# Performance work log

Hardware: AMD Instinct MI355X
Metric: run time of the kernel (lower is better)

The kernel has to match this reference:

```python
import jax, jax.numpy as jnp
import numpy as np

MARGIN = 0.3
WARMUP_EPOCHS = 10
K = 5
ALPHA = 2.0
SAME_CAM_NEG_BOOST = 1.2
NEG_INF = jnp.float32(-jnp.inf)
POS_INF = jnp.float32(jnp.inf)


def setup_inputs() -> dict:
    key = jax.random.key(0)
    k1, k2, k3 = jax.random.split(key, 3)
    N, D = 8192, 2048
    feats = jax.random.normal(k1, (N, D), dtype=jnp.float32)
    labels = jax.random.randint(k2, (N,), 0, 256, dtype=jnp.int64)
    camids = jax.random.randint(k3, (N,), 0, 8, dtype=jnp.int64)
    return {"feats": feats, "labels": labels, "camids": camids, "epoch": 20}


def _topk_mean(dist_mat, mask, k, largest):
    # dist_mat [N,N], mask [N,N] bool. Per-row mean of k largest/smallest valid elems.
    if largest:
        work = jnp.where(mask, dist_mat, NEG_INF)
        vals, _ = jax.lax.top_k(work, k)            # [N,k] largest
        fallback = jnp.max(work, axis=1)
    else:
        work = jnp.where(mask, dist_mat, POS_INF)
        vals = -jax.lax.top_k(-work, k)[0]          # [N,k] smallest
        fallback = jnp.min(work, axis=1)
    is_valid = jnp.isfinite(vals)
    safe_sum = jnp.sum(jnp.where(is_valid, vals, 0.0), axis=1)
    counts = jnp.maximum(is_valid.sum(axis=1), 1)
    mean = safe_sum / counts
    return jnp.where(is_valid.any(axis=1), mean, fallback)


def _forward(feats, labels, camids, epoch):
    # (1) L2 normalize
    norm = jnp.linalg.norm(feats, axis=-1, keepdims=True)
    x = feats / jnp.maximum(norm, 1e-12)
    # Euclidean distance matrix [N,N]
    sq = jnp.sum(x * x, axis=1)
    dist2 = sq[:, None] + sq[None, :] - 2.0 * (x @ x.T)
    dist = jnp.sqrt(jnp.maximum(dist2, 1e-12))
    # masks (constants w.r.t. grad)
    N = feats.shape[0]
    eye = jnp.eye(N, dtype=bool)
    same_label = labels[:, None] == labels[None, :]
    same_cam = camids[:, None] == camids[None, :]
    is_pos = same_label & ~eye & ~same_cam   # cross_cam_pos=True
    is_neg = ~same_label & ~eye
    # boosted same-camera negatives
    neg_bias = jnp.where(is_neg & same_cam, SAME_CAM_NEG_BOOST, 1.0)
    dist_neg_sel = dist / jnp.maximum(neg_bias, 1e-6)
    # (2) top-k hard mining
    d_ap = _topk_mean(dist, is_pos, K, largest=True)
    d_an = _topk_mean(dist_neg_sel, is_neg, K, largest=False)
    # (5) hardness-aware weighting (no grad)
    w = jax.lax.stop_gradient(jax.nn.sigmoid(ALPHA * (d_ap - d_an)))
    w = w / jnp.maximum(w.mean(), 1e-12)
    # (3) margin schedule
    if epoch is not None and epoch < WARMUP_EPOCHS:
        per_sample = jax.nn.softplus(-(d_an - d_ap))
    else:
        per_sample = jax.nn.relu(d_ap - d_an + MARGIN)  # MarginRankingLoss, y=1
    loss = jnp.mean(w * per_sample)
    return loss, jax.lax.stop_gradient(d_ap), jax.lax.stop_gradient(d_an)


def reference(feats, labels, camids, epoch):
    return _forward(feats, labels, camids, epoch)
```

## Files before the change

kernel.cpp:

```cpp
#include <hip/hip_runtime.h>
#include <hip/hip_bf16.h>
#include <stdint.h>

typedef float   floatx4  __attribute__((ext_vector_type(4)));
typedef float   floatx16 __attribute__((ext_vector_type(16)));
typedef int     intx4    __attribute__((ext_vector_type(4)));
typedef int     intx8    __attribute__((ext_vector_type(8)));
typedef _Float16 halfx8  __attribute__((ext_vector_type(8)));
typedef _Float16 halfx4  __attribute__((ext_vector_type(4)));
typedef _Float16 half2v  __attribute__((ext_vector_type(2)));

#define NROW 8192
#define NDIM 2048
#define BM 128
#define SLICE 64
#define NSLICE 32
#define NSTRIP 64
#define NOFF (NSTRIP*(NSTRIP-1)/2)
#define NTILE (NSTRIP*(NSTRIP+1)/2)
#define DT_LD 136
#define KL_SYM 64
#define SLOT_P 8
#define MERGE_BLOCKS 256
#define BOOST_INV 0.6944444444f

__device__ __forceinline__ void ins_desc(float (&a)[5], float v) {
#pragma unroll
    for (int k = 0; k < 5; ++k) { float hi = fmaxf(a[k], v); float lo = fminf(a[k], v); a[k] = hi; v = lo; }
}
__device__ __forceinline__ void ins_asc(float (&a)[5], float v) {
#pragma unroll
    for (int k = 0; k < 5; ++k) { float lo = fminf(a[k], v); float hi = fmaxf(a[k], v); a[k] = lo; v = hi; }
}

__device__ __forceinline__ int   h2bits(half2v v) { return __builtin_bit_cast(int, v); }
__device__ __forceinline__ half2v bits2h(int v)   { return __builtin_bit_cast(half2v, v); }
__device__ __forceinline__ void ins_desc2(half2v (&a)[5], half2v v) {
#pragma unroll
    for (int k = 0; k < 5; ++k) {
        half2v hi = __builtin_elementwise_max(a[k], v);
        half2v lo = __builtin_elementwise_min(a[k], v);
        a[k] = hi; v = lo;
    }
}
__device__ __forceinline__ void ins_asc2(half2v (&a)[5], half2v v) {
#pragma unroll
    for (int k = 0; k < 5; ++k) {
        half2v lo = __builtin_elementwise_min(a[k], v);
        half2v hi = __builtin_elementwise_max(a[k], v);
        a[k] = lo; v = hi;
    }
}

__device__ __forceinline__ void load_lds16(const void* g, void* l) {
    __builtin_amdgcn_global_load_lds((__attribute__((address_space(1))) void*)(void*)g,
                                     (__attribute__((address_space(3))) void*)l,
                                     16, 0, 0);
}

__global__ __launch_bounds__(256) void k_normalize(const float* __restrict__ feats,
                                                   unsigned char* __restrict__ xb,
                                                   float* __restrict__ sq) {
    const int lane = threadIdx.x & 63;
    const int row = (blockIdx.x << 2) + (threadIdx.x >> 6);
    const float* f = feats + (size_t)row * NDIM;
    float4 v[8];
    float ss = 0.f;
#pragma unroll
    for (int i = 0; i < 8; ++i) {
        v[i] = *(const float4*)(f + ((i << 6) + lane) * 4);
        ss += v[i].x * v[i].x + v[i].y * v[i].y + v[i].z * v[i].z + v[i].w * v[i].w;
    }
#pragma unroll
    for (int o = 32; o > 0; o >>= 1) ss += __shfl_xor(ss, o);
    float inv = 1.0f / fmaxf(sqrtf(ss), 1e-12f);
    if (lane == 0) sq[row] = ss * inv * inv;
    unsigned char* xo = xb + (size_t)row * NDIM;
#pragma unroll
    for (int i = 0; i < 8; ++i) {
        int w0 = __builtin_amdgcn_cvt_pk_fp8_f32(v[i].x * inv, v[i].y * inv, 0, false);
        w0     = __builtin_amdgcn_cvt_pk_fp8_f32(v[i].z * inv, v[i].w * inv, w0, true);
        *(int*)(xo + ((i << 6) + lane) * 4) = w0;
    }
}

__device__ __forceinline__ void scan_half_row_neg(const _Float16* Dt_,
        int srow, int shalf, float (&neg5)[5]) {
    const int s2 = 2 * (srow & 7);
    const int PINF2 = 0x7C007C00;
    half2v n5[5];
#pragma unroll
    for (int k = 0; k < 5; ++k) n5[k] = bits2h(PINF2);
#pragma unroll
    for (int c8 = 0; c8 < 8; ++c8) {
        const int pc = ((shalf * 8 + c8) + s2) & 15;
        intx4 v = *(const intx4*)(Dt_ + srow * DT_LD + pc * 8);
#pragma unroll
        for (int e = 0; e < 4; ++e) ins_asc2(n5, bits2h(v[e]));
    }
    half2v tn[5];
#pragma unroll
    for (int k = 0; k < 5; ++k)
        tn[k] = bits2h((int)__builtin_amdgcn_alignbit((unsigned)h2bits(n5[k]), (unsigned)h2bits(n5[k]), 16));
#pragma unroll
    for (int k = 0; k < 5; ++k) ins_asc2(n5, tn[k]);
#pragma unroll
    for (int k = 0; k < 5; ++k) neg5[k] = (float)n5[k][0];
}

__device__ __forceinline__ void emit_neg(float (&neg5)[5], int shalf,
        _Float16* negp, int gi, int slot) {
    float tn[5];
#pragma unroll
    for (int k = 0; k < 5; ++k) tn[k] = __shfl_xor(neg5[k], 1);
#pragma unroll
    for (int k = 0; k < 5; ++k) { if (tn[k] < neg5[4]) ins_asc(neg5, tn[k]); }
    if (shalf == 0) {
        const float PINF = __builtin_inff();
        halfx8 hn;
#pragma unroll
        for (int k = 0; k < 5; ++k) hn[k] = (_Float16)neg5[k];
        hn[5] = hn[6] = hn[7] = (_Float16)PINF;
        *(halfx8*)(negp + ((size_t)slot * NROW + gi) * SLOT_P) = hn;
    }
}

__global__ __launch_bounds__(256, 3) void k_gemm_sym(
        const unsigned char* __restrict__ xb, const float* __restrict__ sq,
        const int* __restrict__ labels, const int* __restrict__ camids,
        _Float16* __restrict__ negp) {
    __shared__ __align__(16) char smem[49152 + 2048];
    _Float16* Dt = (_Float16*)smem;
    float* sqr_s = (float*)(smem + 49152);
    float* sqc_s = sqr_s + BM;
    unsigned short* labcam_a = (unsigned short*)(sqc_s + BM);
    unsigned short* labcam_b = labcam_a + BM;

    const int tid = threadIdx.x;
    const int w = tid >> 6, lane = tid & 63;
    const int wm = w >> 1, wn = w & 1;

    int a, b;
    {
        int bx = blockIdx.x;
        int orig;
        if (bx < NOFF) orig = (bx & 7) * (NOFF / 8) + (bx >> 3);
        else orig = bx;
        if (orig < NOFF) {
            a = (int)((1.0f + sqrtf(8.0f * (float)orig + 1.0f)) * 0.5f);
            while (a * (a - 1) / 2 > orig) --a;
            while (a * (a + 1) / 2 <= orig) ++a;
            b = orig - a * (a - 1) / 2;
        } else {
            a = b = orig - NOFF;
        }
    }
    const int r0 = a * BM, c0 = b * BM;

    const int lr = lane >> 2;
    const int lc = (((lane & 3) - ((lane >> 3) & 3)) & 3) * 16;

    auto stage = [&](int buf, int koff) {
        char* Asb = smem + (buf << 14);
        char* Bsb = Asb + 8192;
#pragma unroll
        for (int q = 0; q < 2; ++q) {
            const int ra = w * 32 + q * 16;
            load_lds16(xb + (size_t)(r0 + ra + lr) * NDIM + koff + lc, Asb + ra * SLICE);
            load_lds16(xb + (size_t)(c0 + ra + lr) * NDIM + koff + lc, Bsb + ra * SLICE);
        }
    };

    if (tid < BM) {
        int gi = r0 + tid;
        sqr_s[tid] = sq[gi];
        labcam_a[tid] = (unsigned short)((labels[gi] << 4) | camids[gi]);
    } else {
        int t2 = tid - BM;
        int gj = c0 + t2;
        sqc_s[t2] = sq[gj];
        labcam_b[t2] = (unsigned short)((labels[gj] << 4) | camids[gj]);
    }

    stage(0, 0);
    stage(1, SLICE);

    const int srow = tid >> 1;
    const int shalf = tid & 1;

    const int m32 = lane & 31;
    const int hi = lane >> 5;
    const int key = (lane >> 1) & 3;
    const int p0 = ((2 * hi + key) & 3) * 16;
    const int p1 = ((2 * hi + 1 + key) & 3) * 16;

    floatx16 acc[2][2];
#pragma unroll
    for (int ti = 0; ti < 2; ++ti)
#pragma unroll
        for (int tj = 0; tj < 2; ++tj)
#pragma unroll
            for (int r = 0; r < 16; ++r) acc[ti][tj][r] = 0.f;

    int bc = 0;
    for (int s = 0; s < NSLICE; ++s) {
        if (s + 2 < NSLICE) {
            int bs = bc + 2; if (bs >= 3) bs -= 3;
            stage(bs, (s + 2) * SLICE);
        }
        if (s < NSLICE - 2)       asm volatile("s_waitcnt vmcnt(8)" ::: "memory");
        else if (s == NSLICE - 2) asm volatile("s_waitcnt vmcnt(4)" ::: "memory");
        else                      asm volatile("s_waitcnt vmcnt(0)" ::: "memory");
        __builtin_amdgcn_s_barrier();
        asm volatile("" ::: "memory");

        const char* Ab = smem + (bc << 14);
        const char* Bb = Ab + 8192;
        intx8 bf[2];
#pragma unroll
        for (int tj = 0; tj < 2; ++tj) {
            const char* bp = Bb + (wn * 64 + tj * 32 + m32) * SLICE;
            intx4 lo = *(const intx4*)(bp + p0);
            intx4 hi4 = *(const intx4*)(bp + p1);
            bf[tj] = __builtin_shufflevector(lo, hi4, 0, 1, 2, 3, 4, 5, 6, 7);
        }
        __builtin_amdgcn_s_setprio(1);
#pragma unroll
        for (int ti = 0; ti < 2; ++ti) {
            const char* ap = Ab + (wm * 64 + ti * 32 + m32) * SLICE;
            intx4 lo = *(const intx4*)(ap + p0);
            intx4 hi4 = *(const intx4*)(ap + p1);
            intx8 af = __builtin_shufflevector(lo, hi4, 0, 1, 2, 3, 4, 5, 6, 7);
            acc[ti][0] = __builtin_amdgcn_mfma_scale_f32_32x32x64_f8f6f4(
                af, bf[0], acc[ti][0], 0, 0, 0, 127, 0, 127);
            acc[ti][1] = __builtin_amdgcn_mfma_scale_f32_32x32x64_f8f6f4(
                af, bf[1], acc[ti][1], 0, 0, 0, 127, 0, 127);
        }
        __builtin_amdgcn_s_setprio(0);
        asm volatile("" ::: "memory");
        __builtin_amdgcn_s_barrier();
        asm volatile("" ::: "memory");
        bc = (bc + 1 == 3) ? 0 : bc + 1;
    }

    const float FINF = __builtin_inff();
#pragma unroll
    for (int ti = 0; ti < 2; ++ti) {
#pragma unroll
        for (int tj = 0; tj < 2; ++tj) {
            const int jl = wn * 64 + tj * 32 + m32;
            const float sj = sqc_s[jl];
            const int lb = (int)labcam_b[jl];
#pragma unroll
            for (int r = 0; r < 16; ++r) {
                const int il = wm * 64 + ti * 32 + (r & 3) + 8 * (r >> 2) + 4 * hi;
                float d2 = fmaxf(sqr_s[il] + sj - 2.0f * acc[ti][tj][r], 1e-12f);
                const int x = (int)labcam_a[il] ^ lb;
                float nv = (x & 15) ? d2 : d2 * BOOST_INV;
                nv = (x & 0xFFF0) ? nv : FINF;
                acc[ti][tj][r] = nv;
                const int pch = ((jl >> 3) + 2 * (il & 7)) & 15;
                Dt[il * DT_LD + (pch << 3) + (jl & 7)] = (_Float16)nv;
            }
        }
    }
    __syncthreads();

    float neg5[5];
    scan_half_row_neg(Dt, srow, shalf, neg5);
    emit_neg(neg5, shalf, negp, r0 + srow, b);

    if (a != b) {
        __syncthreads();
#pragma unroll
        for (int tj = 0; tj < 2; ++tj) {
#pragma unroll
            for (int ti = 0; ti < 2; ++ti) {
                const int jl = wn * 64 + tj * 32 + m32;
                const int cw2 = 2 * (jl & 7);
#pragma unroll
                for (int rq = 0; rq < 4; ++rq) {
                    const int base_row = wm * 64 + ti * 32 + 8 * rq + 4 * hi;
                    halfx4 h;
#pragma unroll
                    for (int e = 0; e < 4; ++e) h[e] = (_Float16)acc[ti][tj][rq * 4 + e];
                    const int pch = (((base_row >> 3) + cw2) & 15);
                    *(halfx4*)(Dt + jl * DT_LD + (pch << 3) + 4 * hi) = h;
                }
            }
        }
        __syncthreads();
        scan_half_row_neg(Dt, srow, shalf, neg5);
        emit_neg(neg5, shalf, negp, c0 + srow, a);
    }
}

__global__ __launch_bounds__(256) void k_pos(const unsigned char* __restrict__ xb,
        const float* __restrict__ sq, const int* __restrict__ labels,
        const int* __restrict__ camids, _Float16* __restrict__ posf) {
    __shared__ int mem[64];
    __shared__ unsigned short mlc[64];
    __shared__ float msq[64];
    __shared__ int cnt_s;
    __shared__ __align__(16) char stg[2][4096];
    __shared__ __align__(16) _Float16 D2[64][72];

    const int t = threadIdx.x, L = blockIdx.x;
    if (t == 0) cnt_s = 0;
    __syncthreads();
    for (int i = t; i < NROW; i += 256) {
        if (labels[i] == L) {
            int slot = atomicAdd(&cnt_s, 1);
            if (slot < 64) mem[slot] = i;
        }
    }
    __syncthreads();
    const int cnt = min(cnt_s, 64);
    if (t < 64) {
        if (t < cnt) {
            int gi = mem[t];
            mlc[t] = (unsigned short)((labels[gi] << 4) | camids[gi]);
            msq[t] = sq[gi];
        } else {
            mem[t] = 0; mlc[t] = 0xFFFF; msq[t] = 0.f;
        }
    }
    __syncthreads();

    const int w = t >> 6, lane = t & 63;
    const int wm = w >> 1, wn = w & 1;
    const int lr = lane >> 2;
    const int lcb = (((lane & 3) - ((lane >> 3) & 3)) & 3) * 16;
    const int m32 = lane & 31, hi = lane >> 5;
    const int key = (lane >> 1) & 3;
    const int p0 = ((2 * hi + key) & 3) * 16;
    const int p1 = ((2 * hi + 1 + key) & 3) * 16;
    const int myrow = mem[w * 16 + lr];

    auto pstage = [&](int buf, int koff) {
        load_lds16(xb + (size_t)myrow * NDIM + koff + lcb, &stg[buf][0] + w * 1024);
    };

    floatx16 acc;
#pragma unroll
    for (int r = 0; r < 16; ++r) acc[r] = 0.f;

    pstage(0, 0);
    __syncthreads();
    for (int s = 0; s < NSLICE; ++s) {
        if (s + 1 < NSLICE) pstage((s + 1) & 1, (s + 1) * SLICE);
        const char* Ab = &stg[s & 1][0];
        const char* ap = Ab + (wm * 32 + m32) * SLICE;
        intx4 alo = *(const intx4*)(ap + p0);
        intx4 ahi = *(const intx4*)(ap + p1);
        intx8 af = __builtin_shufflevector(alo, ahi, 0, 1, 2, 3, 4, 5, 6, 7);
        const char* bp = Ab + (wn * 32 + m32) * SLICE;
        intx4 blo = *(const intx4*)(bp + p0);
        intx4 bhi = *(const intx4*)(bp + p1);
        intx8 bf = __builtin_shufflevector(blo, bhi, 0, 1, 2, 3, 4, 5, 6, 7);
        acc = __builtin_amdgcn_mfma_scale_f32_32x32x64_f8f6f4(af, bf, acc, 0, 0, 0, 127, 0, 127);
        __syncthreads();
    }

    const float NINF = -__builtin_inff();
    {
        const int jl = wn * 32 + m32;
        const int lcj = (int)mlc[jl];
        const float sj = msq[jl];
#pragma unroll
        for (int r = 0; r < 16; ++r) {
            const int il = wm * 32 + (r & 3) + 8 * (r >> 2) + 4 * hi;
            float d2 = fmaxf(msq[il] + sj - 2.0f * acc[r], 1e-12f);
            const int x = (int)mlc[il] ^ lcj;
            bool posv = ((x & 0xFFF0) == 0) & ((x & 15) != 0);
            D2[il][jl] = posv ? (_Float16)d2 : (_Float16)NINF;
        }
    }
    __syncthreads();

    {
        const int prow = t >> 2, q = t & 3;
        const int NINF2 = 0xFC00FC00;
        half2v p5h[5];
#pragma unroll
        for (int k = 0; k < 5; ++k) p5h[k] = bits2h(NINF2);
        const _Float16* dp = &D2[prow][q * 16];
        intx4 v0 = *(const intx4*)dp;
        intx4 v1 = *(const intx4*)(dp + 8);
#pragma unroll
        for (int e = 0; e < 4; ++e) ins_desc2(p5h, bits2h(v0[e]));
#pragma unroll
        for (int e = 0; e < 4; ++e) ins_desc2(p5h, bits2h(v1[e]));
        half2v tp[5];
#pragma unroll
        for (int k = 0; k < 5; ++k)
            tp[k] = bits2h((int)__builtin_amdgcn_alignbit((unsigned)h2bits(p5h[k]), (unsigned)h2bits(p5h[k]), 16));
#pragma unroll
        for (int k = 0; k < 5; ++k) ins_desc2(p5h, tp[k]);
        float p5[5];
#pragma unroll
        for (int k = 0; k < 5; ++k) p5[k] = (float)p5h[k][0];
#pragma unroll
        for (int o = 1; o <= 2; o <<= 1) {
            float tq[5];
#pragma unroll
            for (int k = 0; k < 5; ++k) tq[k] = __shfl_xor(p5[k], o);
#pragma unroll
            for (int k = 0; k < 5; ++k) { if (tq[k] > p5[4]) ins_desc(p5, tq[k]); }
        }
        if (q == 0 && prow < cnt) {
            halfx8 hp;
#pragma unroll
            for (int k = 0; k < 5; ++k) hp[k] = (_Float16)p5[k];
            hp[5] = hp[6] = hp[7] = (_Float16)NINF;
            *(halfx8*)(posf + (size_t)mem[prow] * SLOT_P) = hp;
        }
    }
}

__global__ __launch_bounds__(256) void k_merge_sym(const _Float16* __restrict__ negp,
        const _Float16* __restrict__ posf, const int* __restrict__ epoch_p,
        float* __restrict__ out, float* __restrict__ wsum_p, float* __restrict__ wpsum_p) {
    const int t = threadIdx.x;
    const int rl = t & 31;
    const int sg = t >> 5;
    const int row = blockIdx.x * 32 + rl;
    const float NINF = -__builtin_inff(), PINF = __builtin_inff();
    float n5[5] = {PINF, PINF, PINF, PINF, PINF};
    const size_t rbase = (size_t)row * SLOT_P;
#pragma unroll
    for (int s = 0; s < 8; ++s) {
        const size_t off = (size_t)(sg * 8 + s) * ((size_t)NROW * SLOT_P) + rbase;
        halfx8 nv = *(const halfx8*)(negp + off);
#pragma unroll
        for (int e = 0; e < 8; ++e) { float f = (float)nv[e]; if (f < n5[4]) ins_asc(n5, f); }
    }
    __shared__ __align__(16) _Float16 ln[32][8][8];
    const int sw = (sg + rl) & 7;
    {
        halfx8 hn;
#pragma unroll
        for (int k = 0; k < 5; ++k) hn[k] = (_Float16)n5[k];
        hn[5] = hn[6] = hn[7] = (_Float16)PINF;
        *(halfx8*)&ln[rl][sw][0] = hn;
    }
    __syncthreads();
    if (t < 32) {
        float N5[5] = {PINF, PINF, PINF, PINF, PINF};
#pragma unroll
        for (int g = 0; g < 8; ++g) {
            halfx8 nv = *(const halfx8*)&ln[t][g][0];
#pragma unroll
            for (int e = 0; e < 8; ++e) { float f = (float)nv[e]; if (f < N5[4]) ins_asc(N5, f); }
        }
        const int orow = blockIdx.x * 32 + t;
        halfx8 pv = *(const halfx8*)(posf + (size_t)orow * SLOT_P);
        float s = 0.f; int c = 0;
#pragma unroll
        for (int k = 0; k < 5; ++k) { float f = (float)pv[k]; bool fin = (f > NINF); s += fin ? sqrtf(f) : 0.f; c += fin ? 1 : 0; }
        float d_ap = (c > 0) ? s / (float)c : NINF;
        s = 0.f; c = 0;
#pragma unroll
        for (int k = 0; k < 5; ++k) { bool fin = (N5[k] < PINF); s += fin ? sqrtf(N5[k]) : 0.f; c += fin ? 1 : 0; }
        float d_an = (c > 0) ? s / (float)c : PINF;

        out[1 + orow] = d_ap;
        out[1 + NROW + orow] = d_an;
        float diff = d_ap - d_an;
        float w0 = 1.0f / (1.0f + expf(-2.0f * diff));
        float p;
        if (*epoch_p < 10) {
            p = fmaxf(diff, 0.0f) + log1pf(expf(-fabsf(diff)));
        } else {
            p = fmaxf(diff + 0.3f, 0.0f);
        }
        float wp = w0 * p;
#pragma unroll
        for (int o = 16; o > 0; o >>= 1) { w0 += __shfl_down(w0, o, 32); wp += __shfl_down(wp, o, 32); }
        if (t == 0) { wsum_p[blockIdx.x] = w0; wpsum_p[blockIdx.x] = wp; }
    }
}

__global__ void k_finalize(const float* __restrict__ wsum_p, const float* __restrict__ wpsum_p,
                           float* __restrict__ out) {
    const int t = threadIdx.x;
    float sw  = wsum_p[t] + wsum_p[t + 64] + wsum_p[t + 128] + wsum_p[t + 192];
    float swp = wpsum_p[t] + wpsum_p[t + 64] + wpsum_p[t + 128] + wpsum_p[t + 192];
#pragma unroll
    for (int o = 32; o > 0; o >>= 1) { sw += __shfl_down(sw, o); swp += __shfl_down(swp, o); }
    if (t == 0) {
        float M = fmaxf(sw / (float)NROW, 1e-12f);
        out[0] = swp / ((float)NROW * M);
    }
}

extern "C" void kernel_launch(void* const* d_in, const int* in_sizes, int n_in,
                              void* d_out, int out_size, void* d_ws, size_t ws_size,
                              hipStream_t stream) {
    const float* feats  = (const float*)d_in[0];
    const int*   labels = (const int*)d_in[1];
    const int*   camids = (const int*)d_in[2];
    const int*   epoch  = (const int*)d_in[3];
    float* out = (float*)d_out;
    char* ws = (char*)d_ws;

    unsigned char* xb = (unsigned char*)ws;
    float* sq = (float*)(ws + 16777216);
    const size_t NEG_HALVES = (size_t)KL_SYM * NROW * SLOT_P;
    _Float16* negp = (_Float16*)(ws + 16777216 + 32768);
    _Float16* posf = negp + NEG_HALVES;
    float* wsum_p  = (float*)((char*)(posf + (size_t)NROW * SLOT_P));
    float* wpsum_p = wsum_p + MERGE_BLOCKS;

    k_normalize<<<NROW / 4, 256, 0, stream>>>(feats, xb, sq);
    k_pos<<<256, 256, 0, stream>>>(xb, sq, labels, camids, posf);
    k_gemm_sym<<<NTILE, 256, 0, stream>>>(xb, sq, labels, camids, negp);
    k_merge_sym<<<MERGE_BLOCKS, 256, 0, stream>>>(negp, posf, epoch, out, wsum_p, wpsum_p);
    k_finalize<<<1, 64, 0, stream>>>(wsum_p, wpsum_p, out);
}
```

Before: 227.0 us.

## Fuse positive-pair kernel into symmetric GEMM launch and regroup tiles into 8x8 supertiles

Merges the per-label positive mining kernel into the main symmetric distance GEMM kernel as 256 extra leading blocks, which removes one launch and lets both kinds of work run concurrently. The tile index mapping now groups the 128x128 tiles into 8x8 supertiles, with diagonal supertiles handled separately, to improve L2 reuse of the row strips. The positive path switches to a 3-buffer pipeline with vmcnt waits, and the neg epilogue is restructured to share row loads across the two column subtiles. The cost is that the fused kernel runs at the larger shared-memory footprint and launch bounds of the GEMM path for every block.

```diff
diff --git a/kernel.cpp b/kernel.cpp
--- a/kernel.cpp
+++ b/kernel.cpp
@@ -16,8 +16,8 @@
 #define SLICE 64
 #define NSLICE 32
 #define NSTRIP 64
-#define NOFF (NSTRIP*(NSTRIP-1)/2)
 #define NTILE (NSTRIP*(NSTRIP+1)/2)
+#define NPOSB 256
 #define DT_LD 136
 #define KL_SYM 64
 #define SLOT_P 8
@@ -125,34 +125,181 @@
     }
 }
 
-__global__ __launch_bounds__(256, 3) void k_gemm_sym(
+__global__ __launch_bounds__(256, 3) void k_main(
         const unsigned char* __restrict__ xb, const float* __restrict__ sq,
         const int* __restrict__ labels, const int* __restrict__ camids,
-        _Float16* __restrict__ negp) {
-    __shared__ __align__(16) char smem[49152 + 2048];
+        _Float16* __restrict__ negp, _Float16* __restrict__ posf) {
+    __shared__ __align__(16) char smem[51200];
+
+    const int tid = threadIdx.x;
+    const int w = tid >> 6, lane = tid & 63;
+    const int m32 = lane & 31;
+    const int hi = lane >> 5;
+    const int key = (lane >> 1) & 3;
+    const int p0 = ((2 * hi + key) & 3) * 16;
+    const int p1 = ((2 * hi + 1 + key) & 3) * 16;
+    const float FINF = __builtin_inff();
+    const float NINF = -FINF;
+
+    if (blockIdx.x < NPOSB) {
+        char* stg0 = smem;
+        _Float16* D2 = (_Float16*)(smem + 12288);
+        int* mem = (int*)(smem + 21504);
+        unsigned short* mlc = (unsigned short*)(smem + 21760);
+        float* msq = (float*)(smem + 21888);
+        int* cntp = (int*)(smem + 22144);
+
+        const int L = blockIdx.x;
+        if (tid == 0) *cntp = 0;
+        __syncthreads();
+        for (int i = tid; i < NROW; i += 256) {
+            if (labels[i] == L) {
+                int slot = atomicAdd(cntp, 1);
+                if (slot < 64) mem[slot] = i;
+            }
+        }
+        __syncthreads();
+        const int cnt = min(*cntp, 64);
+        if (tid < 64) {
+            if (tid < cnt) {
+                int gi = mem[tid];
+                mlc[tid] = (unsigned short)((labels[gi] << 4) | camids[gi]);
+                msq[tid] = sq[gi];
+            } else {
+                mem[tid] = 0; mlc[tid] = 0xFFFF; msq[tid] = 0.f;
+            }
+        }
+        __syncthreads();
+
+        const int wm = w >> 1, wn = w & 1;
+        const int lr = lane >> 2;
+        const int lcb = (((lane & 3) - ((lane >> 3) & 3)) & 3) * 16;
+        const int myrow = mem[w * 16 + lr];
+
+        auto pstage = [&](int buf, int koff) {
+            load_lds16(xb + (size_t)myrow * NDIM + koff + lcb,
+                       stg0 + (buf << 12) + w * 1024);
+        };
+
+        floatx16 acc;
+#pragma unroll
+        for (int r = 0; r < 16; ++r) acc[r] = 0.f;
+
+        pstage(0, 0);
+        pstage(1, SLICE);
+        for (int s = 0; s < NSLICE; ++s) {
+            if (s + 2 < NSLICE) {
+                int bs = s + 2; bs -= (bs >= 3 ? 3 : 0); bs -= (bs >= 3 ? 3 : 0);
+                pstage((s + 2) % 3, (s + 2) * SLICE);
+            }
+            if (s < NSLICE - 2)       asm volatile("s_waitcnt vmcnt(2)" ::: "memory");
+            else if (s == NSLICE - 2) asm volatile("s_waitcnt vmcnt(1)" ::: "memory");
+            else                      asm volatile("s_waitcnt vmcnt(0)" ::: "memory");
+            __builtin_amdgcn_s_barrier();
+            asm volatile("" ::: "memory");
+            const char* Ab = stg0 + ((s % 3) << 12);
+            const char* ap = Ab + (wm * 32 + m32) * SLICE;
+            intx4 alo = *(const intx4*)(ap + p0);
+            intx4 ahi = *(const intx4*)(ap + p1);
+            intx8 af = __builtin_shufflevector(alo, ahi, 0, 1, 2, 3, 4, 5, 6, 7);
+            const char* bp = Ab + (wn * 32 + m32) * SLICE;
+            intx4 blo = *(const intx4*)(bp + p0);
+            intx4 bhi = *(const intx4*)(bp + p1);
+            intx8 bf = __builtin_shufflevector(blo, bhi, 0, 1, 2, 3, 4, 5, 6, 7);
+            acc = __builtin_amdgcn_mfma_scale_f32_32x32x64_f8f6f4(af, bf, acc, 0, 0, 0, 127, 0, 127);
+            asm volatile("" ::: "memory");
+            __builtin_amdgcn_s_barrier();
+            asm volatile("" ::: "memory");
+        }
+
+        {
+            const int jl = (w & 1) * 32 + m32;
+            const int lcj = (int)mlc[jl];
+            const float sj = msq[jl];
+            const int wm2 = w >> 1;
+#pragma unroll
+            for (int r = 0; r < 16; ++r) {
+                const int il = wm2 * 32 + (r & 3) + 8 * (r >> 2) + 4 * hi;
+                float d2 = fmaxf(msq[il] + sj - 2.0f * acc[r], 1e-12f);
+                const int x = (int)mlc[il] ^ lcj;
+                bool posv = ((x & 0xFFF0) == 0) & ((x & 15) != 0);
+                D2[il * 72 + jl] = posv ? (_Float16)d2 : (_Float16)NINF;
+            }
+        }
+        __syncthreads();
+
+        {
+            const int prow = tid >> 2, q = tid & 3;
+            const int NINF2 = 0xFC00FC00;
+            half2v p5h[5];
+#pragma unroll
+            for (int k = 0; k < 5; ++k) p5h[k] = bits2h(NINF2);
+            const _Float16* dp = D2 + prow * 72 + q * 16;
+            intx4 v0 = *(const intx4*)dp;
+            intx4 v1 = *(const intx4*)(dp + 8);
+#pragma unroll
+            for (int e = 0; e < 4; ++e) ins_desc2(p5h, bits2h(v0[e]));
+#pragma unroll
+            for (int e = 0; e < 4; ++e) ins_desc2(p5h, bits2h(v1[e]));
+            half2v tp[5];
+#pragma unroll
+            for (int k = 0; k < 5; ++k)
+                tp[k] = bits2h((int)__builtin_amdgcn_alignbit((unsigned)h2bits(p5h[k]), (unsigned)h2bits(p5h[k]), 16));
+#pragma unroll
+            for (int k = 0; k < 5; ++k) ins_desc2(p5h, tp[k]);
+            float p5[5];
+#pragma unroll
+            for (int k = 0; k < 5; ++k) p5[k] = (float)p5h[k][0];
+#pragma unroll
+            for (int o = 1; o <= 2; o <<= 1) {
+                float tq[5];
+#pragma unroll
+                for (int k = 0; k < 5; ++k) tq[k] = __shfl_xor(p5[k], o);
+#pragma unroll
+                for (int k = 0; k < 5; ++k) { if (tq[k] > p5[4]) ins_desc(p5, tq[k]); }
+            }
+            if (q == 0 && prow < cnt) {
+                halfx8 hp;
+#pragma unroll
+                for (int k = 0; k < 5; ++k) hp[k] = (_Float16)p5[k];
+                hp[5] = hp[6] = hp[7] = (_Float16)NINF;
+                *(halfx8*)(posf + (size_t)mem[prow] * SLOT_P) = hp;
+            }
+        }
+        return;
+    }
+
     _Float16* Dt = (_Float16*)smem;
     float* sqr_s = (float*)(smem + 49152);
     float* sqc_s = sqr_s + BM;
     unsigned short* labcam_a = (unsigned short*)(sqc_s + BM);
     unsigned short* labcam_b = labcam_a + BM;
 
-    const int tid = threadIdx.x;
-    const int w = tid >> 6, lane = tid & 63;
     const int wm = w >> 1, wn = w & 1;
 
     int a, b;
     {
-        int bx = blockIdx.x;
-        int orig;
-        if (bx < NOFF) orig = (bx & 7) * (NOFF / 8) + (bx >> 3);
-        else orig = bx;
-        if (orig < NOFF) {
-            a = (int)((1.0f + sqrtf(8.0f * (float)orig + 1.0f)) * 0.5f);
-            while (a * (a - 1) / 2 > orig) --a;
-            while (a * (a + 1) / 2 <= orig) ++a;
-            b = orig - a * (a - 1) / 2;
+        int bx = blockIdx.x - NPOSB;
+        int o = (bx & 7) * (NTILE / 8) + (bx >> 3);
+        if (o < 1792) {
+            int st = o >> 6;
+            int SA = (int)((1.0f + sqrtf(8.0f * (float)st + 1.0f)) * 0.5f);
+            while (SA * (SA - 1) / 2 > st) --SA;
+            while (SA * (SA + 1) / 2 <= st) ++SA;
+            int SB = st - SA * (SA - 1) / 2;
+            int inner = o & 63;
+            a = SA * 8 + (inner >> 3);
+            b = SB * 8 + (inner & 7);
         } else {
-            a = b = orig - NOFF;
+            int idx = o - 1792;
+            int st = idx / 36;
+            int inner = idx - st * 36;
+            int ia = (int)((sqrtf(8.0f * (float)inner + 1.0f) - 1.0f) * 0.5f);
+            while (ia * (ia + 1) / 2 > inner) --ia;
+            while ((ia + 1) * (ia + 2) / 2 <= inner) ++ia;
+            int ib = inner - ia * (ia + 1) / 2;
+            a = st * 8 + ia;
+            b = st * 8 + ib;
         }
     }
     const int r0 = a * BM, c0 = b * BM;
@@ -188,12 +335,6 @@
     const int srow = tid >> 1;
     const int shalf = tid & 1;
 
-    const int m32 = lane & 31;
-    const int hi = lane >> 5;
-    const int key = (lane >> 1) & 3;
-    const int p0 = ((2 * hi + key) & 3) * 16;
-    const int p1 = ((2 * hi + 1 + key) & 3) * 16;
-
     floatx16 acc[2][2];
 #pragma unroll
     for (int ti = 0; ti < 2; ++ti)
@@ -243,24 +384,35 @@
         bc = (bc + 1 == 3) ? 0 : bc + 1;
     }
 
-    const float FINF = __builtin_inff();
-#pragma unroll
-    for (int ti = 0; ti < 2; ++ti) {
-#pragma unroll
-        for (int tj = 0; tj < 2; ++tj) {
-            const int jl = wn * 64 + tj * 32 + m32;
-            const float sj = sqc_s[jl];
-            const int lb = (int)labcam_b[jl];
+    {
+        const int jl0 = wn * 64 + m32, jl1 = jl0 + 32;
+        const float sj0 = sqc_s[jl0], sj1 = sqc_s[jl1];
+        const int lb0 = (int)labcam_b[jl0], lb1 = (int)labcam_b[jl1];
+        const int jc0 = jl0 >> 3, j7_0 = jl0 & 7;
+        const int jc1 = jl1 >> 3, j7_1 = jl1 & 7;
+#pragma unroll
+        for (int ti = 0; ti < 2; ++ti) {
 #pragma unroll
             for (int r = 0; r < 16; ++r) {
                 const int il = wm * 64 + ti * 32 + (r & 3) + 8 * (r >> 2) + 4 * hi;
-                float d2 = fmaxf(sqr_s[il] + sj - 2.0f * acc[ti][tj][r], 1e-12f);
-                const int x = (int)labcam_a[il] ^ lb;
+                const float si = sqr_s[il];
+                const int la = (int)labcam_a[il];
+                const int rot = 2 * (il & 7);
+                _Float16* drow = Dt + il * DT_LD;
+
+                float d2 = fmaxf(si + sj0 - 2.0f * acc[ti][0][r], 1e-12f);
+                int x = la ^ lb0;
                 float nv = (x & 15) ? d2 : d2 * BOOST_INV;
                 nv = (x & 0xFFF0) ? nv : FINF;
-                acc[ti][tj][r] = nv;
-                const int pch = ((jl >> 3) + 2 * (il & 7)) & 15;
-                Dt[il * DT_LD + (pch << 3) + (jl & 7)] = (_Float16)nv;
+                acc[ti][0][r] = nv;
+                drow[(((jc0 + rot) & 15) << 3) + j7_0] = (_Float16)nv;
+
+                d2 = fmaxf(si + sj1 - 2.0f * acc[ti][1][r], 1e-12f);
+                x = la ^ lb1;
+                nv = (x & 15) ? d2 : d2 * BOOST_INV;
+                nv = (x & 0xFFF0) ? nv : FINF;
+                acc[ti][1][r] = nv;
+                drow[(((jc1 + rot) & 15) << 3) + j7_1] = (_Float16)nv;
             }
         }
     }
@@ -292,129 +444,6 @@
         __syncthreads();
         scan_half_row_neg(Dt, srow, shalf, neg5);
         emit_neg(neg5, shalf, negp, c0 + srow, a);
-    }
-}
-
-__global__ __launch_bounds__(256) void k_pos(const unsigned char* __restrict__ xb,
-        const float* __restrict__ sq, const int* __restrict__ labels,
-        const int* __restrict__ camids, _Float16* __restrict__ posf) {
-    __shared__ int mem[64];
-    __shared__ unsigned short mlc[64];
-    __shared__ float msq[64];
-    __shared__ int cnt_s;
-    __shared__ __align__(16) char stg[2][4096];
-    __shared__ __align__(16) _Float16 D2[64][72];
-
-    const int t = threadIdx.x, L = blockIdx.x;
-    if (t == 0) cnt_s = 0;
-    __syncthreads();
-    for (int i = t; i < NROW; i += 256) {
-        if (labels[i] == L) {
-            int slot = atomicAdd(&cnt_s, 1);
-            if (slot < 64) mem[slot] = i;
-        }
-    }
-    __syncthreads();
-    const int cnt = min(cnt_s, 64);
-    if (t < 64) {
-        if (t < cnt) {
-            int gi = mem[t];
-            mlc[t] = (unsigned short)((labels[gi] << 4) | camids[gi]);
-            msq[t] = sq[gi];
-        } else {
-            mem[t] = 0; mlc[t] = 0xFFFF; msq[t] = 0.f;
-        }
-    }
-    __syncthreads();
-
-    const int w = t >> 6, lane = t & 63;
-    const int wm = w >> 1, wn = w & 1;
-    const int lr = lane >> 2;
-    const int lcb = (((lane & 3) - ((lane >> 3) & 3)) & 3) * 16;
-    const int m32 = lane & 31, hi = lane >> 5;
-    const int key = (lane >> 1) & 3;
-    const int p0 = ((2 * hi + key) & 3) * 16;
-    const int p1 = ((2 * hi + 1 + key) & 3) * 16;
-    const int myrow = mem[w * 16 + lr];
-
-    auto pstage = [&](int buf, int koff) {
-        load_lds16(xb + (size_t)myrow * NDIM + koff + lcb, &stg[buf][0] + w * 1024);
-    };
-
-    floatx16 acc;
-#pragma unroll
-    for (int r = 0; r < 16; ++r) acc[r] = 0.f;
-
-    pstage(0, 0);
-    __syncthreads();
-    for (int s = 0; s < NSLICE; ++s) {
-        if (s + 1 < NSLICE) pstage((s + 1) & 1, (s + 1) * SLICE);
-        const char* Ab = &stg[s & 1][0];
-        const char* ap = Ab + (wm * 32 + m32) * SLICE;
-        intx4 alo = *(const intx4*)(ap + p0);
-        intx4 ahi = *(const intx4*)(ap + p1);
-        intx8 af = __builtin_shufflevector(alo, ahi, 0, 1, 2, 3, 4, 5, 6, 7);
-        const char* bp = Ab + (wn * 32 + m32) * SLICE;
-        intx4 blo = *(const intx4*)(bp + p0);
-        intx4 bhi = *(const intx4*)(bp + p1);
-        intx8 bf = __builtin_shufflevector(blo, bhi, 0, 1, 2, 3, 4, 5, 6, 7);
-        acc = __builtin_amdgcn_mfma_scale_f32_32x32x64_f8f6f4(af, bf, acc, 0, 0, 0, 127, 0, 127);
-        __syncthreads();
-    }
-
-    const float NINF = -__builtin_inff();
-    {
-        const int jl = wn * 32 + m32;
-        const int lcj = (int)mlc[jl];
-        const float sj = msq[jl];
-#pragma unroll
-        for (int r = 0; r < 16; ++r) {
-            const int il = wm * 32 + (r & 3) + 8 * (r >> 2) + 4 * hi;
-            float d2 = fmaxf(msq[il] + sj - 2.0f * acc[r], 1e-12f);
-            const int x = (int)mlc[il] ^ lcj;
-            bool posv = ((x & 0xFFF0) == 0) & ((x & 15) != 0);
-            D2[il][jl] = posv ? (_Float16)d2 : (_Float16)NINF;
-        }
-    }
-    __syncthreads();
-
-    {
-        const int prow = t >> 2, q = t & 3;
-        const int NINF2 = 0xFC00FC00;
-        half2v p5h[5];
-#pragma unroll
-        for (int k = 0; k < 5; ++k) p5h[k] = bits2h(NINF2);
-        const _Float16* dp = &D2[prow][q * 16];
-        intx4 v0 = *(const intx4*)dp;
-        intx4 v1 = *(const intx4*)(dp + 8);
-#pragma unroll
-        for (int e = 0; e < 4; ++e) ins_desc2(p5h, bits2h(v0[e]));
-#pragma unroll
-        for (int e = 0; e < 4; ++e) ins_desc2(p5h, bits2h(v1[e]));
-        half2v tp[5];
-#pragma unroll
-        for (int k = 0; k < 5; ++k)
-            tp[k] = bits2h((int)__builtin_amdgcn_alignbit((unsigned)h2bits(p5h[k]), (unsigned)h2bits(p5h[k]), 16));
-#pragma unroll
-        for (int k = 0; k < 5; ++k) ins_desc2(p5h, tp[k]);
-        float p5[5];
-#pragma unroll
-        for (int k = 0; k < 5; ++k) p5[k] = (float)p5h[k][0];
-#pragma unroll
-        for (int o = 1; o <= 2; o <<= 1) {
-            float tq[5];
-#pragma unroll
-            for (int k = 0; k < 5; ++k) tq[k] = __shfl_xor(p5[k], o);
-#pragma unroll
-            for (int k = 0; k < 5; ++k) { if (tq[k] > p5[4]) ins_desc(p5, tq[k]); }
-        }
-        if (q == 0 && prow < cnt) {
-            halfx8 hp;
-#pragma unroll
-            for (int k = 0; k < 5; ++k) hp[k] = (_Float16)p5[k];
-            hp[5] = hp[6] = hp[7] = (_Float16)NINF;
-            *(halfx8*)(posf + (size_t)mem[prow] * SLOT_P) = hp;
-        }
     }
 }
 
@@ -513,8 +542,7 @@
     float* wpsum_p = wsum_p + MERGE_BLOCKS;
 
     k_normalize<<<NROW / 4, 256, 0, stream>>>(feats, xb, sq);
-    k_pos<<<256, 256, 0, stream>>>(xb, sq, labels, camids, posf);
-    k_gemm_sym<<<NTILE, 256, 0, stream>>>(xb, sq, labels, camids, negp);
+    k_main<<<NPOSB + NTILE, 256, 0, stream>>>(xb, sq, labels, camids, negp, posf);
     k_merge_sym<<<MERGE_BLOCKS, 256, 0, stream>>>(negp, posf, epoch, out, wsum_p, wpsum_p);
     k_finalize<<<1, 64, 0, stream>>>(wsum_p, wpsum_p, out);
 }
```

New measurement: 207.5 us. 1.09x faster.
